# Kernel optimization log

Measured on AMD Instinct MI355X. Metric: run time of the kernel, lower is better.

## Reference

```python
import jax, jax.numpy as jnp
import numpy as np

B, L, D, MAX_WIDTH = 8, 512, 768, 12
N = L * MAX_WIDTH  # number of candidate spans


def setup_inputs() -> dict:
    key = jax.random.key(0)
    ks = jax.random.split(key, 5)
    scale = 1.0 / np.sqrt(D)
    h = jax.random.normal(ks[0], (B, L, D), dtype=jnp.float32)
    span_idx = jax.random.randint(ks[1], (B, N, 2), 0, L, dtype=jnp.int64)
    Ws = jax.random.normal(ks[2], (D, D), dtype=jnp.float32) * scale
    We = jax.random.normal(ks[3], (D, D), dtype=jnp.float32) * scale
    Wo = jax.random.normal(ks[4], (2 * D, D), dtype=jnp.float32) * scale
    bs = jnp.zeros((D,), jnp.float32)
    be = jnp.zeros((D,), jnp.float32)
    bo = jnp.zeros((D,), jnp.float32)
    return {"h": h, "span_idx": span_idx, "Ws": Ws, "bs": bs,
            "We": We, "be": be, "Wo": Wo, "bo": bo}


def reference(h, span_idx, Ws, bs, We, be, Wo, bo):
    # project_start / project_end: Linear(D -> D)
    start_rep = jnp.einsum('bld,de->ble', h, Ws) + bs  # (B, L, D)
    end_rep = jnp.einsum('bld,de->ble', h, We) + be    # (B, L, D)
    # gather per-span start/end token representations (irregular access)
    idx_s = span_idx[:, :, 0][:, :, None]  # (B, N, 1)
    idx_e = span_idx[:, :, 1][:, :, None]
    start_span = jnp.take_along_axis(start_rep, idx_s, axis=1)  # (B, N, D)
    end_span = jnp.take_along_axis(end_rep, idx_e, axis=1)      # (B, N, D)
    cat = jax.nn.relu(jnp.concatenate([start_span, end_span], axis=-1))  # (B, N, 2D)
    out = jnp.einsum('bnf,fd->bnd', cat, Wo) + bo  # (B, N, D)
    return out.reshape(B, L, MAX_WIDTH, D)
```

## Files before the change

### kernel.cpp

```cpp
#include <hip/hip_runtime.h>
#include <hip/hip_bf16.h>
#include <stdint.h>


#define Bsz 8
#define Lsz 512
#define Dsz 768
#define Nsz 6144
#define Mrows (Bsz * Lsz)

typedef __attribute__((ext_vector_type(8))) short bf16x8;
typedef __attribute__((ext_vector_type(4))) float f32x4;

#define AS1 __attribute__((address_space(1)))
#define AS3 __attribute__((address_space(3)))

__device__ __forceinline__ void gll16(const void* g, void* l) {
    __builtin_amdgcn_global_load_lds((const AS1 unsigned int*)(uintptr_t)g,
                                     (AS3 unsigned int*)(uintptr_t)l, 16, 0, 0);
}

#define PRE_BLOCKS 5376
__global__ __launch_bounds__(256) void preprocess(const float* __restrict__ h,
                                                  const float* __restrict__ Ws,
                                                  const float* __restrict__ We,
                                                  const float* __restrict__ Wo,
                                                  __hip_bfloat16* __restrict__ hb,
                                                  __hip_bfloat16* __restrict__ Wcat,
                                                  __hip_bfloat16* __restrict__ Wot) {
    int blk = blockIdx.x;
    if (blk < 3072) {
        int i = blk * 256 + threadIdx.x;
        float4 v = reinterpret_cast<const float4*>(h)[i];
        union { __hip_bfloat16 hh[4]; short4 s; } u;
        u.hh[0] = __float2bfloat16(v.x);
        u.hh[1] = __float2bfloat16(v.y);
        u.hh[2] = __float2bfloat16(v.z);
        u.hh[3] = __float2bfloat16(v.w);
        reinterpret_cast<short4*>(hb)[i] = u.s;
        return;
    }
    const float* in;
    __hip_bfloat16* out;
    int R, id;
    if (blk < 3648)      { in = Ws; out = Wcat;                       R = Dsz;     id = blk - 3072; }
    else if (blk < 4224) { in = We; out = Wcat + (size_t)Dsz * Dsz;   R = Dsz;     id = blk - 3648; }
    else                 { in = Wo; out = Wot;                        R = 2 * Dsz; id = blk - 4224; }
    int bx = id % 24, by = id / 24;
    int cb = bx * 32, rb = by * 32;
    __shared__ float tile[32][33];
    int x = threadIdx.x & 31, y0 = threadIdx.x >> 5;
#pragma unroll
    for (int j = 0; j < 4; j++)
        tile[y0 + j * 8][x] = in[(size_t)(rb + y0 + j * 8) * Dsz + cb + x];
    __syncthreads();
#pragma unroll
    for (int j = 0; j < 4; j++)
        out[(size_t)(cb + y0 + j * 8) * R + rb + x] = __float2bfloat16(tile[x][y0 + j * 8]);
}

__device__ __forceinline__ void compute_tile64(const __hip_bfloat16* As, const __hip_bfloat16* Bs,
                                               int lane, int wr, int wc, f32x4 (&acc)[2][4]) {
#pragma unroll
    for (int kk = 0; kk < 64; kk += 32) {
        int ko = kk + 8 * (lane >> 4);
        bf16x8 af[2], bfr[4];
#pragma unroll
        for (int mf = 0; mf < 2; mf++)
            af[mf] = *(const bf16x8*)&As[(wr * 32 + mf * 16 + (lane & 15)) * 64 + ko];
#pragma unroll
        for (int nf = 0; nf < 4; nf++)
            bfr[nf] = *(const bf16x8*)&Bs[(wc * 64 + nf * 16 + (lane & 15)) * 64 + ko];
#pragma unroll
        for (int mf = 0; mf < 2; mf++)
#pragma unroll
            for (int nf = 0; nf < 4; nf++)
                acc[mf][nf] = __builtin_amdgcn_mfma_f32_16x16x32_bf16(af[mf], bfr[nf], acc[mf][nf], 0, 0, 0);
    }
}

__global__ __launch_bounds__(256) void gemm1_relu(const __hip_bfloat16* __restrict__ A,
                                                  const __hip_bfloat16* __restrict__ Bt,
                                                  const float* __restrict__ bs,
                                                  const float* __restrict__ be,
                                                  __hip_bfloat16* __restrict__ C) {
    __shared__ __hip_bfloat16 As[2][64 * 64];
    __shared__ __hip_bfloat16 Bs[2][128 * 64];
    int tid = threadIdx.x, lane = tid & 63, wave = tid >> 6;
    int wr = wave >> 1, wc = wave & 1;
    int m0 = blockIdx.x * 64, n0 = blockIdx.y * 128;
    int r = tid >> 3, c8 = (tid & 7) * 8;

    const __hip_bfloat16* ga[2];
    const __hip_bfloat16* gb[4];
#pragma unroll
    for (int i = 0; i < 2; i++)
        ga[i] = A + (size_t)(m0 + r + i * 32) * Dsz + c8;
#pragma unroll
    for (int i = 0; i < 4; i++)
        gb[i] = Bt + (size_t)(n0 + r + i * 32) * Dsz + c8;

    f32x4 acc[2][4];
#pragma unroll
    for (int mf = 0; mf < 2; mf++)
#pragma unroll
        for (int nf = 0; nf < 4; nf++) acc[mf][nf] = (f32x4){0.f, 0.f, 0.f, 0.f};

#define STAGE1(buf, kt)                                                          \
    do {                                                                         \
        _Pragma("unroll")                                                        \
        for (int i = 0; i < 2; i++) gll16(ga[i] + (kt), &As[buf][(i * 256 + tid) * 8]); \
        _Pragma("unroll")                                                        \
        for (int i = 0; i < 4; i++) gll16(gb[i] + (kt), &Bs[buf][(i * 256 + tid) * 8]); \
    } while (0)

    STAGE1(0, 0);
    __syncthreads();
    int cur = 0;
    for (int t = 0; t < Dsz / 64 - 1; ++t) {
        STAGE1(cur ^ 1, (t + 1) * 64);
        compute_tile64(As[cur], Bs[cur], lane, wr, wc, acc);
        __syncthreads();
        cur ^= 1;
    }
    compute_tile64(As[cur], Bs[cur], lane, wr, wc, acc);
#undef STAGE1

#pragma unroll
    for (int mf = 0; mf < 2; mf++) {
        int r0 = m0 + wr * 32 + mf * 16 + (lane >> 4) * 4;
#pragma unroll
        for (int nf = 0; nf < 4; nf++) {
            int col = n0 + wc * 64 + nf * 16 + (lane & 15);
            float bv = col < Dsz ? bs[col] : be[col - Dsz];
#pragma unroll
            for (int rg = 0; rg < 4; rg++) {
                float v = acc[mf][nf][rg] + bv;
                v = v > 0.f ? v : 0.f;
                C[(size_t)(r0 + rg) * (2 * Dsz) + col] = __float2bfloat16(v);
            }
        }
    }
}

__global__ __launch_bounds__(256) void gemm2_nt(const __hip_bfloat16* __restrict__ SE,
                                                const __hip_bfloat16* __restrict__ Wot,
                                                __hip_bfloat16* __restrict__ P) {
    __shared__ __hip_bfloat16 As[2][64 * 64];
    __shared__ __hip_bfloat16 Bs[2][128 * 64];
    int tid = threadIdx.x, lane = tid & 63, wave = tid >> 6;
    int wr = wave >> 1, wc = wave & 1;
    int m0 = blockIdx.x * 64, n0 = blockIdx.y * 128;
    int z = blockIdx.z;
    int koff = z * Dsz;
    int r = tid >> 3, c8 = (tid & 7) * 8;

    const __hip_bfloat16* ga[2];
    const __hip_bfloat16* gb[4];
#pragma unroll
    for (int i = 0; i < 2; i++)
        ga[i] = SE + (size_t)(m0 + r + i * 32) * (2 * Dsz) + koff + c8;
#pragma unroll
    for (int i = 0; i < 4; i++)
        gb[i] = Wot + (size_t)(n0 + r + i * 32) * (2 * Dsz) + koff + c8;

    f32x4 acc[2][4];
#pragma unroll
    for (int mf = 0; mf < 2; mf++)
#pragma unroll
        for (int nf = 0; nf < 4; nf++) acc[mf][nf] = (f32x4){0.f, 0.f, 0.f, 0.f};

#define STAGE2(buf, kt)                                                          \
    do {                                                                         \
        _Pragma("unroll")                                                        \
        for (int i = 0; i < 2; i++) gll16(ga[i] + (kt), &As[buf][(i * 256 + tid) * 8]); \
        _Pragma("unroll")                                                        \
        for (int i = 0; i < 4; i++) gll16(gb[i] + (kt), &Bs[buf][(i * 256 + tid) * 8]); \
    } while (0)

    STAGE2(0, 0);
    __syncthreads();
    int cur = 0;
    for (int t = 0; t < Dsz / 64 - 1; ++t) {
        STAGE2(cur ^ 1, (t + 1) * 64);
        compute_tile64(As[cur], Bs[cur], lane, wr, wc, acc);
        __syncthreads();
        cur ^= 1;
    }
    compute_tile64(As[cur], Bs[cur], lane, wr, wc, acc);
#undef STAGE2

    __hip_bfloat16* Pz = P + (size_t)z * Mrows * Dsz;
#pragma unroll
    for (int mf = 0; mf < 2; mf++) {
        int r0 = m0 + wr * 32 + mf * 16 + (lane >> 4) * 4;
#pragma unroll
        for (int nf = 0; nf < 4; nf++) {
            int col = n0 + wc * 64 + nf * 16 + (lane & 15);
#pragma unroll
            for (int rg = 0; rg < 4; rg++)
                Pz[(size_t)(r0 + rg) * Dsz + col] = __float2bfloat16(acc[mf][nf][rg]);
        }
    }
}

#define GA_BLOCKS 2304
#define GA_TOT (Bsz * Nsz * 96)
__global__ __launch_bounds__(256) void gather_add(const __hip_bfloat16* __restrict__ P,
                                                  const int* __restrict__ span_idx,
                                                  const float* __restrict__ bo,
                                                  float* __restrict__ out) {
    for (int u = blockIdx.x * 256 + threadIdx.x; u < GA_TOT; u += GA_BLOCKS * 256) {
        int r = u / 96;
        int d = (u % 96) * 8;
        int b = r / Nsz;
        int is = span_idx[2 * r];
        int ie = span_idx[2 * r + 1];
        const bf16x8 p1 = *(const bf16x8*)&P[((size_t)(b * Lsz + is)) * Dsz + d];
        const bf16x8 p2 = *(const bf16x8*)&P[((size_t)(Mrows + b * Lsz + ie)) * Dsz + d];
        f32x4 b0 = *(const f32x4*)&bo[d];
        f32x4 b1 = *(const f32x4*)&bo[d + 4];
        f32x4 o0, o1;
        union { unsigned int u32; float f; } cv;
#define CVT(x) (cv.u32 = ((unsigned int)(unsigned short)(x)) << 16, cv.f)
        o0[0] = CVT(p1[0]) + CVT(p2[0]) + b0[0];
        o0[1] = CVT(p1[1]) + CVT(p2[1]) + b0[1];
        o0[2] = CVT(p1[2]) + CVT(p2[2]) + b0[2];
        o0[3] = CVT(p1[3]) + CVT(p2[3]) + b0[3];
        o1[0] = CVT(p1[4]) + CVT(p2[4]) + b1[0];
        o1[1] = CVT(p1[5]) + CVT(p2[5]) + b1[1];
        o1[2] = CVT(p1[6]) + CVT(p2[6]) + b1[2];
        o1[3] = CVT(p1[7]) + CVT(p2[7]) + b1[3];
#undef CVT
        float* op = &out[(size_t)r * Dsz + d];
        *(f32x4*)op = o0;
        *(f32x4*)(op + 4) = o1;
    }
}

extern "C" void kernel_launch(void* const* d_in, const int* in_sizes, int n_in,
                              void* d_out, int out_size, void* d_ws, size_t ws_size,
                              hipStream_t stream) {
    const float* h        = (const float*)d_in[0];
    const int*   span_idx = (const int*)d_in[1];
    const float* Ws       = (const float*)d_in[2];
    const float* bs       = (const float*)d_in[3];
    const float* We       = (const float*)d_in[4];
    const float* be       = (const float*)d_in[5];
    const float* Wo       = (const float*)d_in[6];
    const float* bo       = (const float*)d_in[7];
    float* out            = (float*)d_out;

    __hip_bfloat16* hb   = (__hip_bfloat16*)d_ws;
    __hip_bfloat16* Wcat = hb + (size_t)Mrows * Dsz;
    __hip_bfloat16* Wot  = Wcat + (size_t)2 * Dsz * Dsz;
    __hip_bfloat16* SE   = Wot + (size_t)Dsz * 2 * Dsz;
    __hip_bfloat16* P    = SE + (size_t)Mrows * 2 * Dsz;

    preprocess<<<PRE_BLOCKS, 256, 0, stream>>>(h, Ws, We, Wo, hb, Wcat, Wot);

    gemm1_relu<<<dim3(Mrows / 64, 2 * Dsz / 128), 256, 0, stream>>>(hb, Wcat, bs, be, SE);

    gemm2_nt<<<dim3(Mrows / 64, Dsz / 128, 2), 256, 0, stream>>>(SE, Wot, P);

    gather_add<<<GA_BLOCKS, 256, 0, stream>>>(P, span_idx, bo, out);
}
```

Measured before the change: 88.59 us.

## Triple-buffer GEMM LDS tiles with partial vmcnt waits for deeper prefetch

Both GEMM kernels move from a double-buffered LDS pipeline with full __syncthreads to a three-stage ring buffer. Two tiles are prefetched ahead, and only the oldest tile's loads are waited on via s_waitcnt vmcnt(6) before a raw s_barrier. The aim is to hide global-to-LDS latency behind more MFMA work per barrier. LDS use rises from 48KB to 72KB per block, which can lower occupancy. The fully unrolled 12-iteration loop also grows code size.

```diff
diff --git a/kernel.cpp b/kernel.cpp
--- a/kernel.cpp
+++ b/kernel.cpp
@@ -8,6 +8,7 @@
 #define Dsz 768
 #define Nsz 6144
 #define Mrows (Bsz * Lsz)
+#define NT (Dsz / 64)
 
 typedef __attribute__((ext_vector_type(8))) short bf16x8;
 typedef __attribute__((ext_vector_type(4))) float f32x4;
@@ -19,6 +20,10 @@
     __builtin_amdgcn_global_load_lds((const AS1 unsigned int*)(uintptr_t)g,
                                      (AS3 unsigned int*)(uintptr_t)l, 16, 0, 0);
 }
+
+#define VMWAIT6() asm volatile("s_waitcnt vmcnt(6)" ::: "memory")
+#define VMWAIT0() asm volatile("s_waitcnt vmcnt(0)" ::: "memory")
+#define BARRIER() do { __builtin_amdgcn_s_barrier(); __builtin_amdgcn_sched_barrier(0); } while (0)
 
 #define PRE_BLOCKS 5376
 __global__ __launch_bounds__(256) void preprocess(const float* __restrict__ h,
@@ -84,8 +89,8 @@
                                                   const float* __restrict__ bs,
                                                   const float* __restrict__ be,
                                                   __hip_bfloat16* __restrict__ C) {
-    __shared__ __hip_bfloat16 As[2][64 * 64];
-    __shared__ __hip_bfloat16 Bs[2][128 * 64];
+    __shared__ __hip_bfloat16 As[3][64 * 64];
+    __shared__ __hip_bfloat16 Bs[3][128 * 64];
     int tid = threadIdx.x, lane = tid & 63, wave = tid >> 6;
     int wr = wave >> 1, wc = wave & 1;
     int m0 = blockIdx.x * 64, n0 = blockIdx.y * 128;
@@ -115,15 +120,18 @@
     } while (0)
 
     STAGE1(0, 0);
-    __syncthreads();
-    int cur = 0;
-    for (int t = 0; t < Dsz / 64 - 1; ++t) {
-        STAGE1(cur ^ 1, (t + 1) * 64);
-        compute_tile64(As[cur], Bs[cur], lane, wr, wc, acc);
-        __syncthreads();
-        cur ^= 1;
-    }
-    compute_tile64(As[cur], Bs[cur], lane, wr, wc, acc);
+    STAGE1(1, 64);
+    VMWAIT6();
+    BARRIER();
+#pragma unroll
+    for (int t = 0; t < NT; ++t) {
+        if (t + 2 < NT) STAGE1((t + 2) % 3, (t + 2) * 64);
+        compute_tile64(As[t % 3], Bs[t % 3], lane, wr, wc, acc);
+        if (t < NT - 1) {
+            if (t + 2 < NT) VMWAIT6(); else VMWAIT0();
+            BARRIER();
+        }
+    }
 #undef STAGE1
 
 #pragma unroll
@@ -146,8 +154,8 @@
 __global__ __launch_bounds__(256) void gemm2_nt(const __hip_bfloat16* __restrict__ SE,
                                                 const __hip_bfloat16* __restrict__ Wot,
                                                 __hip_bfloat16* __restrict__ P) {
-    __shared__ __hip_bfloat16 As[2][64 * 64];
-    __shared__ __hip_bfloat16 Bs[2][128 * 64];
+    __shared__ __hip_bfloat16 As[3][64 * 64];
+    __shared__ __hip_bfloat16 Bs[3][128 * 64];
     int tid = threadIdx.x, lane = tid & 63, wave = tid >> 6;
     int wr = wave >> 1, wc = wave & 1;
     int m0 = blockIdx.x * 64, n0 = blockIdx.y * 128;
@@ -179,15 +187,18 @@
     } while (0)
 
     STAGE2(0, 0);
-    __syncthreads();
-    int cur = 0;
-    for (int t = 0; t < Dsz / 64 - 1; ++t) {
-        STAGE2(cur ^ 1, (t + 1) * 64);
-        compute_tile64(As[cur], Bs[cur], lane, wr, wc, acc);
-        __syncthreads();
-        cur ^= 1;
-    }
-    compute_tile64(As[cur], Bs[cur], lane, wr, wc, acc);
+    STAGE2(1, 64);
+    VMWAIT6();
+    BARRIER();
+#pragma unroll
+    for (int t = 0; t < NT; ++t) {
+        if (t + 2 < NT) STAGE2((t + 2) % 3, (t + 2) * 64);
+        compute_tile64(As[t % 3], Bs[t % 3], lane, wr, wc, acc);
+        if (t < NT - 1) {
+            if (t + 2 < NT) VMWAIT6(); else VMWAIT0();
+            BARRIER();
+        }
+    }
 #undef STAGE2
 
     __hip_bfloat16* Pz = P + (size_t)z * Mrows * Dsz;
```

New measurement: 90.63 us. 2.3% more time.
